# Optimization experiments

Hardware: AMD Instinct MI355X
Metric: run time of the kernel (lower is better)

## Reference

```python
import jax, jax.numpy as jnp
import numpy as np

# tinygemm asymmetric int4 convention
QUANT_MIN, QUANT_MAX = 0, 15
MID_POINT = (QUANT_MAX + QUANT_MIN + 1) / 2.0  # 8.0
OUT_F, IN_F, GROUP = 8192, 8192, 128
M_TOKENS = 64


def setup_inputs() -> dict:
    key = jax.random.key(0)
    kx, kw = jax.random.split(key)
    x = jax.random.normal(kx, (M_TOKENS, IN_F), dtype=jnp.float32)
    # Materialize quantized params exactly as quantize_weight_tinygemm does.
    w = jax.random.normal(kw, (OUT_F, IN_F), dtype=jnp.float32) * 0.02
    ng = IN_F // GROUP
    wg = w.reshape(OUT_F, ng, GROUP)
    min_val = wg.min(axis=2)
    max_val = wg.max(axis=2)
    scale = jnp.maximum((max_val - min_val) / float(QUANT_MAX - QUANT_MIN), 1.1920929e-7)
    zero_point = min_val + scale * MID_POINT
    min_val_recon = zero_point - scale * MID_POINT
    q = jnp.clip(jnp.round((wg - min_val_recon[..., None]) / scale[..., None]),
                 QUANT_MIN, QUANT_MAX).astype(jnp.int32)
    int_data = q.reshape(OUT_F, IN_F)  # values in [0, 15]
    # tinygemm layout: (n_groups, out_features, 2) with [..., 0]=scale, [..., 1]=zero_point
    scale_and_zero = jnp.stack([scale, zero_point], axis=-1).transpose(1, 0, 2)
    return {"x": x, "int_data": int_data, "scale_and_zero": scale_and_zero}


def reference(x, int_data, scale_and_zero):
    # Dequant: w = (q - MID_POINT) * scale + zero_point, per group of GROUP along in_features.
    ng = IN_F // GROUP
    q = int_data.reshape(OUT_F, ng, GROUP).astype(x.dtype)
    scale = scale_and_zero[..., 0].T[:, :, None]       # (OUT_F, ng, 1)
    zero_point = scale_and_zero[..., 1].T[:, :, None]  # (OUT_F, ng, 1)
    w = ((q - MID_POINT) * scale + zero_point).reshape(OUT_F, IN_F)
    return x @ w.T  # (M, OUT_F)
```

## Files before the change

### kernel.cpp

```cpp
#include <hip/hip_runtime.h>
#include <hip/hip_bf16.h>


#define OUT_F 8192
#define IN_F  8192
#define M_TOK 64
#define GROUP 128
#define BN    64
#define KSPLIT 8
#define KR    (IN_F / KSPLIT)
#define GROUPS (KR / GROUP)

typedef short short8 __attribute__((ext_vector_type(8)));
typedef float f32x4  __attribute__((ext_vector_type(4)));
typedef unsigned u32x4 __attribute__((ext_vector_type(4)));

__device__ __forceinline__ unsigned pk(float lo, float hi) {
    __hip_bfloat162 h = __float22bfloat162_rn(float2{lo, hi});
    unsigned r;
    __builtin_memcpy(&r, &h, sizeof(r));
    return r;
}

__global__ void zero_out(float* __restrict__ p) {
    const int i = (blockIdx.x * 256 + threadIdx.x) * 4;
    *(float4*)(p + i) = float4{0.f, 0.f, 0.f, 0.f};
}

__global__ __launch_bounds__(256, 4)
void woq_gemm(const float* __restrict__ x,
              const int*   __restrict__ qw,
              const float* __restrict__ sz,
              float*       __restrict__ outp) {
    __shared__ int lds_x[2][1024 * 4];

    const int t    = threadIdx.x;
    const int lane = t & 63;
    const int wv   = t >> 6;
    const int n0   = blockIdx.x * BN;
    const int k0   = blockIdx.y * KR;

    const int nlo  = lane & 15;
    const int quad = lane >> 4;
    const int kq8  = quad << 3;

    const int n1 = n0 + wv * 16 + nlo;
    const int* qr = qw + (size_t)n1 * IN_F;

    f32x4 acc[4];
#pragma unroll
    for (int mi = 0; mi < 4; ++mi) acc[mi] = (f32x4){0.f, 0.f, 0.f, 0.f};

    float4 xs[8];

#pragma unroll
    for (int i = 0; i < 4; ++i) {
        const int slot  = t + 256 * i;
        const int chunk = slot >> 6;
        const int l     = slot & 63;
        const int m     = ((chunk & 3) << 4) + (l & 15);
        const int kk    = ((chunk >> 2) << 5) + ((l >> 4) << 3);
        const float4* p = (const float4*)(x + (size_t)m * IN_F + k0 + kk);
        xs[2 * i]     = p[0];
        xs[2 * i + 1] = p[1];
    }
#pragma unroll
    for (int i = 0; i < 4; ++i) {
        const int slot = t + 256 * i;
        u32x4 bv;
        bv.x = pk(xs[2 * i].x,     xs[2 * i].y);
        bv.y = pk(xs[2 * i].z,     xs[2 * i].w);
        bv.z = pk(xs[2 * i + 1].x, xs[2 * i + 1].y);
        bv.w = pk(xs[2 * i + 1].z, xs[2 * i + 1].w);
        *(u32x4*)&lds_x[0][slot * 4] = bv;
    }
    __syncthreads();

    for (int g = 0; g < GROUPS; ++g) {
        const int kg = k0 + g * GROUP;

        if (g + 1 < GROUPS) {
#pragma unroll
            for (int i = 0; i < 4; ++i) {
                const int slot  = t + 256 * i;
                const int chunk = slot >> 6;
                const int l     = slot & 63;
                const int m     = ((chunk & 3) << 4) + (l & 15);
                const int kk    = ((chunk >> 2) << 5) + ((l >> 4) << 3);
                const float4* p = (const float4*)(x + (size_t)m * IN_F + kg + GROUP + kk);
                xs[2 * i]     = p[0];
                xs[2 * i + 1] = p[1];
            }
        }

        const int gg = kg >> 7;
        const float2 ps = *(const float2*)(sz + ((size_t)gg * OUT_F + n1) * 2);
        const float s1 = ps.x, c1 = fmaf(-8.f, ps.x, ps.y);
        const int* bufp = lds_x[g & 1];

#pragma unroll
        for (int ks = 0; ks < 4; ++ks) {
            const int* qp = qr + kg + ks * 32 + kq8;
            const int4 qa = *(const int4*)(qp);
            const int4 qb = *(const int4*)(qp + 4);

            short8 a[4];
#pragma unroll
            for (int mi = 0; mi < 4; ++mi)
                a[mi] = *(const short8*)&bufp[((ks * 4 + mi) * 64 + lane) * 4];

            u32x4 bi;
            bi.x = pk(fmaf((float)qa.x, s1, c1), fmaf((float)qa.y, s1, c1));
            bi.y = pk(fmaf((float)qa.z, s1, c1), fmaf((float)qa.w, s1, c1));
            bi.z = pk(fmaf((float)qb.x, s1, c1), fmaf((float)qb.y, s1, c1));
            bi.w = pk(fmaf((float)qb.z, s1, c1), fmaf((float)qb.w, s1, c1));
            const short8 b = __builtin_bit_cast(short8, bi);

#pragma unroll
            for (int mi = 0; mi < 4; ++mi)
                acc[mi] = __builtin_amdgcn_mfma_f32_16x16x32_bf16(a[mi], b, acc[mi], 0, 0, 0);
        }

        if (g + 1 < GROUPS) {
            int* dstb = lds_x[(g + 1) & 1];
#pragma unroll
            for (int i = 0; i < 4; ++i) {
                const int slot = t + 256 * i;
                u32x4 bv;
                bv.x = pk(xs[2 * i].x,     xs[2 * i].y);
                bv.y = pk(xs[2 * i].z,     xs[2 * i].w);
                bv.z = pk(xs[2 * i + 1].x, xs[2 * i + 1].y);
                bv.w = pk(xs[2 * i + 1].z, xs[2 * i + 1].w);
                *(u32x4*)&dstb[slot * 4] = bv;
            }
            __syncthreads();
        }
    }

#pragma unroll
    for (int mi = 0; mi < 4; ++mi) {
#pragma unroll
        for (int r = 0; r < 4; ++r) {
            const int m = mi * 16 + quad * 4 + r;
            atomicAdd(outp + (size_t)m * OUT_F + n1, acc[mi][r]);
        }
    }
}

extern "C" void kernel_launch(void* const* d_in, const int* in_sizes, int n_in,
                              void* d_out, int out_size, void* d_ws, size_t ws_size,
                              hipStream_t stream) {
    const float* x  = (const float*)d_in[0];
    const int*   qw = (const int*)d_in[1];
    const float* sz = (const float*)d_in[2];
    float* out = (float*)d_out;

    zero_out<<<dim3((M_TOK * OUT_F) / (256 * 4)), 256, 0, stream>>>(out);
    woq_gemm<<<dim3(OUT_F / BN, KSPLIT), 256, 0, stream>>>(x, qw, sz, out);
}
```

Baseline: 394.6 us.

## Stage dequantized weights through LDS with coalesced loads and intra-block k-split reduction

```diff
diff --git a/kernel.cpp b/kernel.cpp
--- a/kernel.cpp
+++ b/kernel.cpp
@@ -7,13 +7,12 @@
 #define M_TOK 64
 #define GROUP 128
 #define BN    64
-#define KSPLIT 8
+#define KSPLIT 4
 #define KR    (IN_F / KSPLIT)
 #define GROUPS (KR / GROUP)
 
 typedef short short8 __attribute__((ext_vector_type(8)));
 typedef float f32x4  __attribute__((ext_vector_type(4)));
-typedef unsigned u32x4 __attribute__((ext_vector_type(4)));
 
 __device__ __forceinline__ unsigned pk(float lo, float hi) {
     __hip_bfloat162 h = __float22bfloat162_rn(float2{lo, hi});
@@ -27,123 +26,136 @@
     *(float4*)(p + i) = float4{0.f, 0.f, 0.f, 0.f};
 }
 
-__global__ __launch_bounds__(256, 4)
+__global__ __launch_bounds__(512, 4)
 void woq_gemm(const float* __restrict__ x,
               const int*   __restrict__ qw,
               const float* __restrict__ sz,
               float*       __restrict__ outp) {
-    __shared__ int lds_x[2][1024 * 4];
+    __shared__ int lds_x[2][4096];
+    __shared__ int lds_w[2][4096];
 
     const int t    = threadIdx.x;
     const int lane = t & 63;
     const int wv   = t >> 6;
+    const int wn   = wv & 3;
+    const int kh   = wv >> 2;
     const int n0   = blockIdx.x * BN;
     const int k0   = blockIdx.y * KR;
 
     const int nlo  = lane & 15;
     const int quad = lane >> 4;
-    const int kq8  = quad << 3;
+    const int row  = wn * 16 + nlo;
+    const int n1   = n0 + row;
 
-    const int n1 = n0 + wv * 16 + nlo;
-    const int* qr = qw + (size_t)n1 * IN_F;
+    const int tr = t >> 5;
+    const int kc = t & 31;
 
     f32x4 acc[4];
 #pragma unroll
     for (int mi = 0; mi < 4; ++mi) acc[mi] = (f32x4){0.f, 0.f, 0.f, 0.f};
 
-    float4 xs[8];
+    int4   wq[4];
+    float2 sc[4];
+    float4 xs[4];
 
+    auto stage_load = [&](int g) {
+        const int kg = k0 + g * GROUP;
 #pragma unroll
-    for (int i = 0; i < 4; ++i) {
-        const int slot  = t + 256 * i;
-        const int chunk = slot >> 6;
-        const int l     = slot & 63;
-        const int m     = ((chunk & 3) << 4) + (l & 15);
-        const int kk    = ((chunk >> 2) << 5) + ((l >> 4) << 3);
-        const float4* p = (const float4*)(x + (size_t)m * IN_F + k0 + kk);
-        xs[2 * i]     = p[0];
-        xs[2 * i + 1] = p[1];
-    }
+        for (int i = 0; i < 4; ++i) {
+            const int r = i * 16 + tr;
+            wq[i] = *(const int4*)(qw + (size_t)(n0 + r) * IN_F + kg + kc * 4);
+        }
+        const int gg = kg >> 7;
 #pragma unroll
-    for (int i = 0; i < 4; ++i) {
-        const int slot = t + 256 * i;
-        u32x4 bv;
-        bv.x = pk(xs[2 * i].x,     xs[2 * i].y);
-        bv.y = pk(xs[2 * i].z,     xs[2 * i].w);
-        bv.z = pk(xs[2 * i + 1].x, xs[2 * i + 1].y);
-        bv.w = pk(xs[2 * i + 1].z, xs[2 * i + 1].w);
-        *(u32x4*)&lds_x[0][slot * 4] = bv;
-    }
+        for (int i = 0; i < 4; ++i) {
+            const int r = i * 16 + tr;
+            sc[i] = *(const float2*)(sz + ((size_t)gg * OUT_F + n0 + r) * 2);
+        }
+#pragma unroll
+        for (int j = 0; j < 2; ++j) {
+            const int slot  = t + 512 * j;
+            const int chunk = slot >> 6;
+            const int l     = slot & 63;
+            const int m     = ((chunk & 3) << 4) + (l & 15);
+            const int kk    = ((chunk >> 2) << 5) + ((l >> 4) << 3);
+            const float4* p = (const float4*)(x + (size_t)m * IN_F + kg + kk);
+            xs[2 * j]     = p[0];
+            xs[2 * j + 1] = p[1];
+        }
+    };
+
+    auto stage_write = [&](int buf) {
+        int* wb = lds_w[buf];
+#pragma unroll
+        for (int i = 0; i < 4; ++i) {
+            const int r = i * 16 + tr;
+            const float s = sc[i].x;
+            const float c = fmaf(-8.f, sc[i].x, sc[i].y);
+            int2 v;
+            v.x = (int)pk(fmaf((float)wq[i].x, s, c), fmaf((float)wq[i].y, s, c));
+            v.y = (int)pk(fmaf((float)wq[i].z, s, c), fmaf((float)wq[i].w, s, c));
+            const int idx = (r * 64 + kc * 2) ^ ((r & 7) << 2);
+            *(int2*)&wb[idx] = v;
+        }
+        int* xb = lds_x[buf];
+#pragma unroll
+        for (int j = 0; j < 2; ++j) {
+            const int slot = t + 512 * j;
+            int4 bv;
+            bv.x = (int)pk(xs[2 * j].x,     xs[2 * j].y);
+            bv.y = (int)pk(xs[2 * j].z,     xs[2 * j].w);
+            bv.z = (int)pk(xs[2 * j + 1].x, xs[2 * j + 1].y);
+            bv.w = (int)pk(xs[2 * j + 1].z, xs[2 * j + 1].w);
+            *(int4*)&xb[slot * 4] = bv;
+        }
+    };
+
+    stage_load(0);
+    stage_write(0);
     __syncthreads();
 
     for (int g = 0; g < GROUPS; ++g) {
-        const int kg = k0 + g * GROUP;
+        if (g + 1 < GROUPS) stage_load(g + 1);
 
-        if (g + 1 < GROUPS) {
+        const int* xb = lds_x[g & 1];
+        const int* wb = lds_w[g & 1];
 #pragma unroll
-            for (int i = 0; i < 4; ++i) {
-                const int slot  = t + 256 * i;
-                const int chunk = slot >> 6;
-                const int l     = slot & 63;
-                const int m     = ((chunk & 3) << 4) + (l & 15);
-                const int kk    = ((chunk >> 2) << 5) + ((l >> 4) << 3);
-                const float4* p = (const float4*)(x + (size_t)m * IN_F + kg + GROUP + kk);
-                xs[2 * i]     = p[0];
-                xs[2 * i + 1] = p[1];
-            }
-        }
-
-        const int gg = kg >> 7;
-        const float2 ps = *(const float2*)(sz + ((size_t)gg * OUT_F + n1) * 2);
-        const float s1 = ps.x, c1 = fmaf(-8.f, ps.x, ps.y);
-        const int* bufp = lds_x[g & 1];
-
-#pragma unroll
-        for (int ks = 0; ks < 4; ++ks) {
-            const int* qp = qr + kg + ks * 32 + kq8;
-            const int4 qa = *(const int4*)(qp);
-            const int4 qb = *(const int4*)(qp + 4);
-
+        for (int s = 0; s < 2; ++s) {
+            const int ks = kh * 2 + s;
+            const int bidx = (row * 64 + ks * 16 + quad * 4) ^ ((row & 7) << 2);
+            const short8 b = *(const short8*)&wb[bidx];
             short8 a[4];
 #pragma unroll
             for (int mi = 0; mi < 4; ++mi)
-                a[mi] = *(const short8*)&bufp[((ks * 4 + mi) * 64 + lane) * 4];
-
-            u32x4 bi;
-            bi.x = pk(fmaf((float)qa.x, s1, c1), fmaf((float)qa.y, s1, c1));
-            bi.y = pk(fmaf((float)qa.z, s1, c1), fmaf((float)qa.w, s1, c1));
-            bi.z = pk(fmaf((float)qb.x, s1, c1), fmaf((float)qb.y, s1, c1));
-            bi.w = pk(fmaf((float)qb.z, s1, c1), fmaf((float)qb.w, s1, c1));
-            const short8 b = __builtin_bit_cast(short8, bi);
-
+                a[mi] = *(const short8*)&xb[((ks * 4 + mi) * 64 + lane) * 4];
 #pragma unroll
             for (int mi = 0; mi < 4; ++mi)
                 acc[mi] = __builtin_amdgcn_mfma_f32_16x16x32_bf16(a[mi], b, acc[mi], 0, 0, 0);
         }
 
         if (g + 1 < GROUPS) {
-            int* dstb = lds_x[(g + 1) & 1];
-#pragma unroll
-            for (int i = 0; i < 4; ++i) {
-                const int slot = t + 256 * i;
-                u32x4 bv;
-                bv.x = pk(xs[2 * i].x,     xs[2 * i].y);
-                bv.y = pk(xs[2 * i].z,     xs[2 * i].w);
-                bv.z = pk(xs[2 * i + 1].x, xs[2 * i + 1].y);
-                bv.w = pk(xs[2 * i + 1].z, xs[2 * i + 1].w);
-                *(u32x4*)&dstb[slot * 4] = bv;
-            }
+            stage_write((g + 1) & 1);
             __syncthreads();
         }
     }
 
+    __syncthreads();
+    f32x4* redp = (f32x4*)&lds_x[0][0];
+    if (kh == 1) {
 #pragma unroll
-    for (int mi = 0; mi < 4; ++mi) {
+        for (int mi = 0; mi < 4; ++mi)
+            redp[(wn * 4 + mi) * 64 + lane] = acc[mi];
+    }
+    __syncthreads();
+    if (kh == 0) {
 #pragma unroll
-        for (int r = 0; r < 4; ++r) {
-            const int m = mi * 16 + quad * 4 + r;
-            atomicAdd(outp + (size_t)m * OUT_F + n1, acc[mi][r]);
-        }
+        for (int mi = 0; mi < 4; ++mi)
+            acc[mi] += redp[(wn * 4 + mi) * 64 + lane];
+#pragma unroll
+        for (int mi = 0; mi < 4; ++mi)
+#pragma unroll
+            for (int r = 0; r < 4; ++r)
+                atomicAdd(outp + (size_t)(mi * 16 + quad * 4 + r) * OUT_F + n1, acc[mi][r]);
     }
 }
 
@@ -156,5 +168,5 @@
     float* out = (float*)d_out;
 
     zero_out<<<dim3((M_TOK * OUT_F) / (256 * 4)), 256, 0, stream>>>(out);
-    woq_gemm<<<dim3(OUT_F / BN, KSPLIT), 256, 0, stream>>>(x, qw, sz, out);
+    woq_gemm<<<dim3(OUT_F / BN, KSPLIT), 512, 0, stream>>>(x, qw, sz, out);
 }
```

Result: faster. 376.3 us (-4.6%).

## Repack int32 weights to 4-bit nibbles before GEMM to cut weight loads

Applied to the files above, without the earlier changes.

```diff
diff --git a/kernel.cpp b/kernel.cpp
--- a/kernel.cpp
+++ b/kernel.cpp
@@ -10,6 +10,7 @@
 #define KSPLIT 8
 #define KR    (IN_F / KSPLIT)
 #define GROUPS (KR / GROUP)
+#define PACK_BYTES ((size_t)OUT_F * IN_F / 2)
 
 typedef short short8 __attribute__((ext_vector_type(8)));
 typedef float f32x4  __attribute__((ext_vector_type(4)));
@@ -27,9 +28,23 @@
     *(float4*)(p + i) = float4{0.f, 0.f, 0.f, 0.f};
 }
 
+__global__ __launch_bounds__(256)
+void repack(const int* __restrict__ qw, unsigned short* __restrict__ pw) {
+    const size_t nth = (size_t)gridDim.x * 256;
+    const int4* q4 = (const int4*)qw;
+    for (size_t i = (size_t)blockIdx.x * 256 + threadIdx.x;
+         i < (size_t)OUT_F * IN_F / 4; i += nth) {
+        const int4 a = q4[i];
+        pw[i] = (unsigned short)((a.x & 15) | ((a.y & 15) << 4) |
+                                 ((a.z & 15) << 8) | ((a.w & 15) << 12));
+    }
+}
+
+template <bool PACKED>
 __global__ __launch_bounds__(256, 4)
 void woq_gemm(const float* __restrict__ x,
               const int*   __restrict__ qw,
+              const unsigned* __restrict__ pw,
               const float* __restrict__ sz,
               float*       __restrict__ outp) {
     __shared__ int lds_x[2][1024 * 4];
@@ -45,7 +60,8 @@
     const int kq8  = quad << 3;
 
     const int n1 = n0 + wv * 16 + nlo;
-    const int* qr = qw + (size_t)n1 * IN_F;
+    const int*      qr  = qw + (size_t)n1 * IN_F;
+    const unsigned* pwr = pw + (size_t)n1 * (IN_F / 8);
 
     f32x4 acc[4];
 #pragma unroll
@@ -100,20 +116,31 @@
 
 #pragma unroll
         for (int ks = 0; ks < 4; ++ks) {
-            const int* qp = qr + kg + ks * 32 + kq8;
-            const int4 qa = *(const int4*)(qp);
-            const int4 qb = *(const int4*)(qp + 4);
-
             short8 a[4];
 #pragma unroll
             for (int mi = 0; mi < 4; ++mi)
                 a[mi] = *(const short8*)&bufp[((ks * 4 + mi) * 64 + lane) * 4];
 
             u32x4 bi;
-            bi.x = pk(fmaf((float)qa.x, s1, c1), fmaf((float)qa.y, s1, c1));
-            bi.y = pk(fmaf((float)qa.z, s1, c1), fmaf((float)qa.w, s1, c1));
-            bi.z = pk(fmaf((float)qb.x, s1, c1), fmaf((float)qb.y, s1, c1));
-            bi.w = pk(fmaf((float)qb.z, s1, c1), fmaf((float)qb.w, s1, c1));
+            if constexpr (PACKED) {
+                const unsigned wb = pwr[(kg + ks * 32 + kq8) >> 3];
+                bi.x = pk(fmaf((float)( wb        & 15u), s1, c1),
+                          fmaf((float)((wb >>  4) & 15u), s1, c1));
+                bi.y = pk(fmaf((float)((wb >>  8) & 15u), s1, c1),
+                          fmaf((float)((wb >> 12) & 15u), s1, c1));
+                bi.z = pk(fmaf((float)((wb >> 16) & 15u), s1, c1),
+                          fmaf((float)((wb >> 20) & 15u), s1, c1));
+                bi.w = pk(fmaf((float)((wb >> 24) & 15u), s1, c1),
+                          fmaf((float)( wb >> 28       ), s1, c1));
+            } else {
+                const int* qp = qr + kg + ks * 32 + kq8;
+                const int4 qa = *(const int4*)(qp);
+                const int4 qb = *(const int4*)(qp + 4);
+                bi.x = pk(fmaf((float)qa.x, s1, c1), fmaf((float)qa.y, s1, c1));
+                bi.y = pk(fmaf((float)qa.z, s1, c1), fmaf((float)qa.w, s1, c1));
+                bi.z = pk(fmaf((float)qb.x, s1, c1), fmaf((float)qb.y, s1, c1));
+                bi.w = pk(fmaf((float)qb.z, s1, c1), fmaf((float)qb.w, s1, c1));
+            }
             const short8 b = __builtin_bit_cast(short8, bi);
 
 #pragma unroll
@@ -156,5 +183,14 @@
     float* out = (float*)d_out;
 
     zero_out<<<dim3((M_TOK * OUT_F) / (256 * 4)), 256, 0, stream>>>(out);
-    woq_gemm<<<dim3(OUT_F / BN, KSPLIT), 256, 0, stream>>>(x, qw, sz, out);
+
+    if (ws_size >= PACK_BYTES) {
+        unsigned short* pw = (unsigned short*)d_ws;
+        repack<<<dim3(2048), 256, 0, stream>>>(qw, pw);
+        woq_gemm<true><<<dim3(OUT_F / BN, KSPLIT), 256, 0, stream>>>(
+            x, qw, (const unsigned*)pw, sz, out);
+    } else {
+        woq_gemm<false><<<dim3(OUT_F / BN, KSPLIT), 256, 0, stream>>>(
+            x, qw, nullptr, sz, out);
+    }
 }
```

After: 423.1 us. 7.2% more time.
